# Performance work log

Measured on AMD Instinct MI355X. Metric: run time of the kernel, lower is better.

The kernel has to match this reference:

```python
import jax, jax.numpy as jnp
import numpy as np

D_MODEL = 1024
D_K = 64
D_V = 64
TEMPERATURE = float(np.sqrt(D_K))
LN_EPS = 1e-5


def setup_inputs() -> dict:
    key = jax.random.key(0)
    ks = jax.random.split(key, 8)
    B, L = 8, 2048
    q = jax.random.normal(ks[0], (B, L, D_K), dtype=jnp.float32)
    k = jax.random.normal(ks[1], (B, L, D_K), dtype=jnp.float32)
    v = jax.random.normal(ks[2], (B, L, D_V), dtype=jnp.float32)
    residual = jax.random.normal(ks[3], (B, L, D_MODEL), dtype=jnp.float32)
    # fc: Linear(d_v, d_model), xavier-normal weight, zero-ish bias
    fc_w = jax.random.normal(ks[4], (D_MODEL, D_V), dtype=jnp.float32) * float(np.sqrt(2.0 / (D_V + D_MODEL)))
    fc_b = jnp.zeros((D_MODEL,), dtype=jnp.float32)
    ln_gamma = jnp.ones((D_MODEL,), dtype=jnp.float32)
    ln_beta = jnp.zeros((D_MODEL,), dtype=jnp.float32)
    return {"q": q, "k": k, "v": v, "residual": residual,
            "fc_w": fc_w, "fc_b": fc_b, "ln_gamma": ln_gamma, "ln_beta": ln_beta}


def reference(q, k, v, residual, fc_w, fc_b, ln_gamma, ln_beta):
    # scaled dot-product attention: scores [B, Lq, Lk]
    scores = jnp.einsum("bqd,bkd->bqk", q, k) / TEMPERATURE
    # module computes both log_softmax and softmax (shared logsumexp in a
    # fused kernel); log_attn is discarded by Attention.forward
    log_attn = jax.nn.log_softmax(scores, axis=2)
    attn = jnp.exp(log_attn)  # == softmax(scores); dropout is identity at eval
    out = jnp.einsum("bqk,bkv->bqv", attn, v)  # [B, Lq, d_v]
    # fc + residual + LayerNorm (dropout identity at eval)
    out = jnp.einsum("bqv,mv->bqm", out, fc_w) + fc_b
    x = out + residual
    mu = jnp.mean(x, axis=-1, keepdims=True)
    var = jnp.var(x, axis=-1, keepdims=True)
    return (x - mu) * jax.lax.rsqrt(var + LN_EPS) * ln_gamma + ln_beta
```

## Files before the change

kernel.cpp:

```cpp
#include <hip/hip_runtime.h>

typedef float  f32x4 __attribute__((ext_vector_type(4)));
typedef float  f4v   __attribute__((ext_vector_type(4)));
typedef short  s16x8 __attribute__((ext_vector_type(8)));
typedef unsigned short u16x4 __attribute__((ext_vector_type(4)));
typedef unsigned short u16x8 __attribute__((ext_vector_type(8)));
typedef unsigned short u16;

#define DEVI static __device__ __forceinline__
#define AS1 __attribute__((address_space(1)))
#define AS3 __attribute__((address_space(3)))

DEVI u16 f2bf(float f) {
  unsigned int u = __builtin_bit_cast(unsigned int, f);
  u += 0x7FFFu + ((u >> 16) & 1u);
  return (u16)(u >> 16);
}

constexpr int B  = 8;
constexpr int L  = 2048;
constexpr int D  = 64;
constexpr int DM = 1024;

__global__ void prep_kernel(const float* __restrict__ k, const float* __restrict__ v,
                            const float* __restrict__ w,
                            u16* __restrict__ kbf, u16* __restrict__ vtbf,
                            u16* __restrict__ wbf) {
  __shared__ float tile[64 * 65];
  const int bid = blockIdx.x, tid = threadIdx.x;
  if (bid < 1024) {
    const int i = bid * 256 + tid;
    f4v f = ((const f4v*)k)[i];
    u16x4 o;
#pragma unroll
    for (int j = 0; j < 4; ++j) o[j] = f2bf(f[j] * 0.125f);
    ((u16x4*)kbf)[i] = o;
  } else if (bid < 1024 + 64) {
    const int i = (bid - 1024) * 256 + tid;
    f4v f = ((const f4v*)w)[i];
    u16x4 o;
#pragma unroll
    for (int j = 0; j < 4; ++j) o[j] = f2bf(f[j]);
    ((u16x4*)wbf)[i] = o;
  } else {
    const int t2 = bid - 1088;
    const int b = t2 >> 5, tt = t2 & 31;
    const float* vp = v + ((size_t)b * L + tt * 64) * D;
    for (int i = tid; i < 4096; i += 256) {
      const int r = i >> 6, c = i & 63;
      tile[c * 65 + r] = vp[i];
    }
    __syncthreads();
    u16* op = vtbf + (size_t)b * D * L + tt * 64;
    for (int i = tid; i < 4096; i += 256) {
      const int dv = i >> 6, kv = i & 63;
      op[(size_t)dv * L + kv] = f2bf(tile[dv * 65 + kv]);
    }
  }
}

__global__ __launch_bounds__(512) void attn_kernel(const float* __restrict__ q,
                                                   const u16* __restrict__ kbf,
                                                   const u16* __restrict__ vtbf,
                                                   u16* __restrict__ Og) {
  const int blk = blockIdx.x;
  const int b = blk >> 5;
  const int qrow0 = (blk & 31) * 64;
  const int tid = threadIdx.x;
  const int wave = tid >> 6, lane = tid & 63;
  const int g = wave >> 1, h = wave & 1;
  const int lg = lane >> 4, ln = lane & 15;

  __shared__ __align__(16) u16   Kt[2][64 * 64];
  __shared__ __align__(16) u16   Vt[2][64 * 64];
  __shared__ __align__(16) u16   Pl[8][16 * 40];
  __shared__ float Macc[8][16][68];
  __shared__ float Lsum[8][16];

  s16x8 aq[2];
  {
    const float* qp = q + ((size_t)b * L + qrow0 + g * 16 + ln) * D + lg * 8;
#pragma unroll
    for (int kk = 0; kk < 2; ++kk) {
      f4v f0 = *(const f4v*)(qp + kk * 32);
      f4v f1 = *(const f4v*)(qp + kk * 32 + 4);
      s16x8 a;
#pragma unroll
      for (int j = 0; j < 4; ++j) { a[j] = (short)f2bf(f0[j]); a[4 + j] = (short)f2bf(f1[j]); }
      aq[kk] = a;
    }
  }

  const f32x4 zf = {0.f, 0.f, 0.f, 0.f};
  f32x4 acc[4];
#pragma unroll
  for (int i = 0; i < 4; ++i) acc[i] = zf;
  float lrow[4] = {0.f, 0.f, 0.f, 0.f};

  const u16* kb = kbf + (size_t)b * L * D;
  const u16* vb = vtbf + (size_t)b * D * L;

  auto stage = [&](int buf, int t) {
    const int kv0 = t * 64;
    const int row = tid >> 3, jl = tid & 7;
    const int js = jl ^ (row & 7);
    const u16* srcK = kb + (size_t)(kv0 + row) * D + js * 8;
    __builtin_amdgcn_global_load_lds(
        (const AS1 unsigned int*)srcK, (AS3 unsigned int*)&Kt[buf][tid * 8], 16, 0, 0);
    const u16* srcV = vb + (size_t)row * L + kv0 + js * 8;
    __builtin_amdgcn_global_load_lds(
        (const AS1 unsigned int*)srcV, (AS3 unsigned int*)&Vt[buf][tid * 8], 16, 0, 0);
  };

  stage(0, 0);

  for (int t = 0; t < 32; ++t) {
    __syncthreads();
    if (t + 1 < 32) stage((t + 1) & 1, t + 1);
    const int buf = t & 1;

    f32x4 s[2];
    s[0] = zf; s[1] = zf;
#pragma unroll
    for (int kk = 0; kk < 2; ++kk) {
#pragma unroll
      for (int fn2 = 0; fn2 < 2; ++fn2) {
        const int kvr = h * 32 + fn2 * 16 + ln;
        const int j = (kk * 4 + lg) ^ (kvr & 7);
        s16x8 bk = *(const s16x8*)&Kt[buf][kvr * 64 + j * 8];
        s[fn2] = __builtin_amdgcn_mfma_f32_16x16x32_bf16(aq[kk], bk, s[fn2], 0, 0, 0);
      }
    }

#pragma unroll
    for (int r = 0; r < 4; ++r) {
      const float p0 = __expf(s[0][r]);
      const float p1 = __expf(s[1][r]);
      lrow[r] += p0 + p1;
      Pl[wave][(lg * 4 + r) * 40 + ln]      = f2bf(p0);
      Pl[wave][(lg * 4 + r) * 40 + 16 + ln] = f2bf(p1);
    }

    asm volatile("" ::: "memory");

    s16x8 ap = *(const s16x8*)&Pl[wave][ln * 40 + lg * 8];
#pragma unroll
    for (int fn = 0; fn < 4; ++fn) {
      const int dv = fn * 16 + ln;
      const int j = (h * 4 + lg) ^ (dv & 7);
      s16x8 bv = *(const s16x8*)&Vt[buf][dv * 64 + j * 8];
      acc[fn] = __builtin_amdgcn_mfma_f32_16x16x32_bf16(ap, bv, acc[fn], 0, 0, 0);
    }
  }

#pragma unroll
  for (int r = 0; r < 4; ++r) {
#pragma unroll
    for (int off = 1; off < 16; off <<= 1) lrow[r] += __shfl_xor(lrow[r], off, 64);
    if (ln == 0) Lsum[wave][lg * 4 + r] = lrow[r];
  }
#pragma unroll
  for (int fn = 0; fn < 4; ++fn)
#pragma unroll
    for (int r = 0; r < 4; ++r)
      Macc[wave][lg * 4 + r][fn * 16 + ln] = acc[fn][r];
  __syncthreads();

  {
    const int row = tid >> 3, d0 = (tid & 7) * 8;
    const int g2 = row >> 4, r2 = row & 15;
    const float linv = 1.f / (Lsum[g2 * 2][r2] + Lsum[g2 * 2 + 1][r2]);
    f4v o0 = *(const f4v*)&Macc[g2 * 2][r2][d0]     + *(const f4v*)&Macc[g2 * 2 + 1][r2][d0];
    f4v o1 = *(const f4v*)&Macc[g2 * 2][r2][d0 + 4] + *(const f4v*)&Macc[g2 * 2 + 1][r2][d0 + 4];
    u16x8 ob;
#pragma unroll
    for (int j = 0; j < 4; ++j) {
      ob[j]     = f2bf(o0[j] * linv);
      ob[4 + j] = f2bf(o1[j] * linv);
    }
    *(u16x8*)(Og + ((size_t)b * L + qrow0 + row) * D + d0) = ob;
  }
}

__global__ __launch_bounds__(512, 2) void fc_ln_kernel(const u16* __restrict__ Og,
                                                       const u16* __restrict__ wbf,
                                                       const float* __restrict__ bias,
                                                       const float* __restrict__ resid,
                                                       const float* __restrict__ gamma,
                                                       const float* __restrict__ beta,
                                                       float* __restrict__ out) {
  __shared__ __align__(16) u16   Wl[1024 * 64];
  __shared__ __align__(16) float bl[1024];
  __shared__ __align__(16) float gl[1024];
  __shared__ __align__(16) float btl[1024];
  __shared__ float part[8][16][2];

  const int tid = threadIdx.x;
  const int wave = tid >> 6, lane = tid & 63;
  const int rg = wave >> 2, mq = wave & 3;
  const int lg = lane >> 4, ln = lane & 15;
  const int m0 = mq * 256;
  const int rowA = blockIdx.x * 64 + rg * 16 + ln;
  const int rowB = rowA + 32;
  const int jb = ln & 7;

  {
#pragma unroll
    for (int i = 0; i < 16; ++i) {
      const int c = tid + i * 512;
      const int r = c >> 3, j = c & 7;
      const u16* src = wbf + r * 64 + (j ^ (r & 7)) * 8;
      __builtin_amdgcn_global_load_lds(
          (const AS1 unsigned int*)src, (AS3 unsigned int*)&Wl[c * 8], 16, 0, 0);
    }
    if (tid < 256) {
      __builtin_amdgcn_global_load_lds(
          (const AS1 unsigned int*)(bias + tid * 4), (AS3 unsigned int*)&bl[tid * 4], 16, 0, 0);
      __builtin_amdgcn_global_load_lds(
          (const AS1 unsigned int*)(beta + tid * 4), (AS3 unsigned int*)&btl[tid * 4], 16, 0, 0);
    } else {
      const int t2 = tid - 256;
      __builtin_amdgcn_global_load_lds(
          (const AS1 unsigned int*)(gamma + t2 * 4), (AS3 unsigned int*)&gl[t2 * 4], 16, 0, 0);
    }
  }

  f4v boAr0, boAr1;
  {
    const u16* opA = Og + (size_t)rowA * D + lg * 8;
    asm volatile("global_load_dwordx4 %0, %1, off"           : "=v"(boAr0) : "v"(opA) : "memory");
    asm volatile("global_load_dwordx4 %0, %1, off offset:64" : "=v"(boAr1) : "v"(opA) : "memory");
  }
  f4v rsdA[16];
  {
    const float* rp = resid + (size_t)rowA * DM + m0 + lg * 4;
#pragma unroll
    for (int fn = 0; fn < 16; ++fn)
      asm volatile("global_load_dwordx4 %0, %1, off offset:%c2"
                   : "=v"(rsdA[fn]) : "v"(rp), "i"(fn * 64) : "memory");
  }

  asm volatile("s_waitcnt vmcnt(0)" ::: "memory");
  __builtin_amdgcn_sched_barrier(0);
  __builtin_amdgcn_s_barrier();
  __builtin_amdgcn_sched_barrier(0);

  f32x4 acc[16];
#pragma unroll
  for (int fn = 0; fn < 16; ++fn)
    acc[fn] = *(const f4v*)&bl[m0 + fn * 16 + lg * 4] + rsdA[fn];

  f4v boBr0, boBr1;
  {
    const u16* opB = Og + (size_t)rowB * D + lg * 8;
    asm volatile("global_load_dwordx4 %0, %1, off"           : "=v"(boBr0) : "v"(opB) : "memory");
    asm volatile("global_load_dwordx4 %0, %1, off offset:64" : "=v"(boBr1) : "v"(opB) : "memory");
  }
  f4v rsdB[16];
  {
    const float* rp = resid + (size_t)rowB * DM + m0 + lg * 4;
#pragma unroll
    for (int fn = 0; fn < 16; ++fn)
      asm volatile("global_load_dwordx4 %0, %1, off offset:%c2"
                   : "=v"(rsdB[fn]) : "v"(rp), "i"(fn * 64) : "memory");
  }

  {
    const s16x8 bo0 = __builtin_bit_cast(s16x8, boAr0);
    const s16x8 bo1 = __builtin_bit_cast(s16x8, boAr1);
#pragma unroll
    for (int fn = 0; fn < 16; ++fn) {
      const int m = m0 + fn * 16 + ln;
      s16x8 aw0 = *(const s16x8*)&Wl[m * 64 + (lg ^ jb) * 8];
      s16x8 aw1 = *(const s16x8*)&Wl[m * 64 + ((4 + lg) ^ jb) * 8];
      acc[fn] = __builtin_amdgcn_mfma_f32_16x16x32_bf16(aw0, bo0, acc[fn], 0, 0, 0);
      acc[fn] = __builtin_amdgcn_mfma_f32_16x16x32_bf16(aw1, bo1, acc[fn], 0, 0, 0);
    }
    float sum = 0.f, ssq = 0.f;
#pragma unroll
    for (int fn = 0; fn < 16; ++fn)
#pragma unroll
      for (int r = 0; r < 4; ++r) { const float x = acc[fn][r]; sum += x; ssq += x * x; }
    sum += __shfl_xor(sum, 16, 64); ssq += __shfl_xor(ssq, 16, 64);
    sum += __shfl_xor(sum, 32, 64); ssq += __shfl_xor(ssq, 32, 64);
    if (lg == 0) { part[wave][ln][0] = sum; part[wave][ln][1] = ssq; }
    asm volatile("s_waitcnt lgkmcnt(0)" ::: "memory");
    __builtin_amdgcn_s_barrier();
    __builtin_amdgcn_sched_barrier(0);
    float sm = 0.f, q2 = 0.f;
#pragma unroll
    for (int w2 = 0; w2 < 4; ++w2) { sm += part[rg * 4 + w2][ln][0]; q2 += part[rg * 4 + w2][ln][1]; }
    const float mu   = sm * (1.0f / 1024.0f);
    const float var  = q2 * (1.0f / 1024.0f) - mu * mu;
    const float rstd = rsqrtf(var + 1e-5f);
#pragma unroll
    for (int fn = 0; fn < 16; ++fn) {
      const int m4 = m0 + fn * 16 + lg * 4;
      const f4v gm = *(const f4v*)&gl[m4];
      const f4v bt = *(const f4v*)&btl[m4];
      f4v o;
#pragma unroll
      for (int r = 0; r < 4; ++r) o[r] = (acc[fn][r] - mu) * rstd * gm[r] + bt[r];
      *(f4v*)&out[(size_t)rowA * DM + m4] = o;
    }
  }

  asm volatile("s_waitcnt vmcnt(0)" ::: "memory");
  __builtin_amdgcn_sched_barrier(0);
  __builtin_amdgcn_s_barrier();
  __builtin_amdgcn_sched_barrier(0);

  {
#pragma unroll
    for (int fn = 0; fn < 16; ++fn)
      acc[fn] = *(const f4v*)&bl[m0 + fn * 16 + lg * 4] + rsdB[fn];
    const s16x8 bo0 = __builtin_bit_cast(s16x8, boBr0);
    const s16x8 bo1 = __builtin_bit_cast(s16x8, boBr1);
#pragma unroll
    for (int fn = 0; fn < 16; ++fn) {
      const int m = m0 + fn * 16 + ln;
      s16x8 aw0 = *(const s16x8*)&Wl[m * 64 + (lg ^ jb) * 8];
      s16x8 aw1 = *(const s16x8*)&Wl[m * 64 + ((4 + lg) ^ jb) * 8];
      acc[fn] = __builtin_amdgcn_mfma_f32_16x16x32_bf16(aw0, bo0, acc[fn], 0, 0, 0);
      acc[fn] = __builtin_amdgcn_mfma_f32_16x16x32_bf16(aw1, bo1, acc[fn], 0, 0, 0);
    }
    float sum = 0.f, ssq = 0.f;
#pragma unroll
    for (int fn = 0; fn < 16; ++fn)
#pragma unroll
      for (int r = 0; r < 4; ++r) { const float x = acc[fn][r]; sum += x; ssq += x * x; }
    sum += __shfl_xor(sum, 16, 64); ssq += __shfl_xor(ssq, 16, 64);
    sum += __shfl_xor(sum, 32, 64); ssq += __shfl_xor(ssq, 32, 64);
    if (lg == 0) { part[wave][ln][0] = sum; part[wave][ln][1] = ssq; }
    asm volatile("s_waitcnt lgkmcnt(0)" ::: "memory");
    __builtin_amdgcn_s_barrier();
    __builtin_amdgcn_sched_barrier(0);
    float sm = 0.f, q2 = 0.f;
#pragma unroll
    for (int w2 = 0; w2 < 4; ++w2) { sm += part[rg * 4 + w2][ln][0]; q2 += part[rg * 4 + w2][ln][1]; }
    const float mu   = sm * (1.0f / 1024.0f);
    const float var  = q2 * (1.0f / 1024.0f) - mu * mu;
    const float rstd = rsqrtf(var + 1e-5f);
#pragma unroll
    for (int fn = 0; fn < 16; ++fn) {
      const int m4 = m0 + fn * 16 + lg * 4;
      const f4v gm = *(const f4v*)&gl[m4];
      const f4v bt = *(const f4v*)&btl[m4];
      f4v o;
#pragma unroll
      for (int r = 0; r < 4; ++r) o[r] = (acc[fn][r] - mu) * rstd * gm[r] + bt[r];
      *(f4v*)&out[(size_t)rowB * DM + m4] = o;
    }
  }
}

extern "C" void kernel_launch(void* const* d_in, const int* in_sizes, int n_in,
                              void* d_out, int out_size, void* d_ws, size_t ws_size,
                              hipStream_t stream) {
  const float* q     = (const float*)d_in[0];
  const float* k     = (const float*)d_in[1];
  const float* v     = (const float*)d_in[2];
  const float* resid = (const float*)d_in[3];
  const float* fc_w  = (const float*)d_in[4];
  const float* fc_b  = (const float*)d_in[5];
  const float* gamma = (const float*)d_in[6];
  const float* beta  = (const float*)d_in[7];
  float* out = (float*)d_out;

  char* ws = (char*)d_ws;
  u16*   kbf  = (u16*)(ws);
  u16*   vtbf = (u16*)(ws + (2u << 20));
  u16*   wbf  = (u16*)(ws + (4u << 20));
  u16*   Og   = (u16*)(ws + (4u << 20) + (128u << 10));

  prep_kernel<<<1344, 256, 0, stream>>>(k, v, fc_w, kbf, vtbf, wbf);
  attn_kernel<<<256, 512, 0, stream>>>(q, kbf, vtbf, Og);
  fc_ln_kernel<<<256, 512, 0, stream>>>(Og, wbf, fc_b, resid, gamma, beta, out);
}
```

Measured before the change: 64.13 us.

## Triple-buffer K/V tiles with vmcnt waits and alias epilogue LDS

Moves the attention kernel's K/V staging from a double buffer to a triple buffer that prefetches two tiles ahead. Each iteration waits on vmcnt and a raw s_barrier, so the wait covers only the older loads rather than a full __syncthreads. The epilogue Macc/Lsum scratch is aliased over the K/V buffers in one shared byte array to keep LDS usage near 58 KB. This aims to hide global load latency better, but relies on hand-written vmcnt counts matching the issued loads, and the extra barrier before the epilogue guards the aliasing.

```diff
diff --git a/kernel.cpp b/kernel.cpp
--- a/kernel.cpp
+++ b/kernel.cpp
@@ -63,6 +63,13 @@
                                                    const u16* __restrict__ kbf,
                                                    const u16* __restrict__ vtbf,
                                                    u16* __restrict__ Og) {
+  __shared__ __align__(16) char smem[58 * 1024];
+  u16*   Kt   = (u16*)smem;
+  u16*   Vt   = (u16*)(smem + 24 * 1024);
+  u16*   Pl   = (u16*)(smem + 48 * 1024);
+  float* Macc = (float*)smem;
+  float* Lsum = (float*)(smem + 35 * 1024);
+
   const int blk = blockIdx.x;
   const int b = blk >> 5;
   const int qrow0 = (blk & 31) * 64;
@@ -71,12 +78,6 @@
   const int g = wave >> 1, h = wave & 1;
   const int lg = lane >> 4, ln = lane & 15;
 
-  __shared__ __align__(16) u16   Kt[2][64 * 64];
-  __shared__ __align__(16) u16   Vt[2][64 * 64];
-  __shared__ __align__(16) u16   Pl[8][16 * 40];
-  __shared__ float Macc[8][16][68];
-  __shared__ float Lsum[8][16];
-
   s16x8 aq[2];
   {
     const float* qp = q + ((size_t)b * L + qrow0 + g * 16 + ln) * D + lg * 8;
@@ -100,24 +101,30 @@
   const u16* kb = kbf + (size_t)b * L * D;
   const u16* vb = vtbf + (size_t)b * D * L;
 
-  auto stage = [&](int buf, int t) {
+  auto stage = [&](int t) {
+    const int buf = t % 3;
     const int kv0 = t * 64;
     const int row = tid >> 3, jl = tid & 7;
     const int js = jl ^ (row & 7);
     const u16* srcK = kb + (size_t)(kv0 + row) * D + js * 8;
     __builtin_amdgcn_global_load_lds(
-        (const AS1 unsigned int*)srcK, (AS3 unsigned int*)&Kt[buf][tid * 8], 16, 0, 0);
+        (const AS1 unsigned int*)srcK, (AS3 unsigned int*)&Kt[buf * 4096 + tid * 8], 16, 0, 0);
     const u16* srcV = vb + (size_t)row * L + kv0 + js * 8;
     __builtin_amdgcn_global_load_lds(
-        (const AS1 unsigned int*)srcV, (AS3 unsigned int*)&Vt[buf][tid * 8], 16, 0, 0);
+        (const AS1 unsigned int*)srcV, (AS3 unsigned int*)&Vt[buf * 4096 + tid * 8], 16, 0, 0);
   };
 
-  stage(0, 0);
+  stage(0);
+  stage(1);
 
   for (int t = 0; t < 32; ++t) {
-    __syncthreads();
-    if (t + 1 < 32) stage((t + 1) & 1, t + 1);
-    const int buf = t & 1;
+    if (t < 31) { asm volatile("s_waitcnt vmcnt(2)" ::: "memory"); }
+    else        { asm volatile("s_waitcnt vmcnt(0)" ::: "memory"); }
+    __builtin_amdgcn_sched_barrier(0);
+    __builtin_amdgcn_s_barrier();
+    __builtin_amdgcn_sched_barrier(0);
+    if (t + 2 < 32) stage(t + 2);
+    const int buf = t % 3;
 
     f32x4 s[2];
     s[0] = zf; s[1] = zf;
@@ -127,7 +134,7 @@
       for (int fn2 = 0; fn2 < 2; ++fn2) {
         const int kvr = h * 32 + fn2 * 16 + ln;
         const int j = (kk * 4 + lg) ^ (kvr & 7);
-        s16x8 bk = *(const s16x8*)&Kt[buf][kvr * 64 + j * 8];
+        s16x8 bk = *(const s16x8*)&Kt[buf * 4096 + kvr * 64 + j * 8];
         s[fn2] = __builtin_amdgcn_mfma_f32_16x16x32_bf16(aq[kk], bk, s[fn2], 0, 0, 0);
       }
     }
@@ -137,41 +144,45 @@
       const float p0 = __expf(s[0][r]);
       const float p1 = __expf(s[1][r]);
       lrow[r] += p0 + p1;
-      Pl[wave][(lg * 4 + r) * 40 + ln]      = f2bf(p0);
-      Pl[wave][(lg * 4 + r) * 40 + 16 + ln] = f2bf(p1);
+      Pl[wave * 640 + (lg * 4 + r) * 40 + ln]      = f2bf(p0);
+      Pl[wave * 640 + (lg * 4 + r) * 40 + 16 + ln] = f2bf(p1);
     }
 
     asm volatile("" ::: "memory");
 
-    s16x8 ap = *(const s16x8*)&Pl[wave][ln * 40 + lg * 8];
+    s16x8 ap = *(const s16x8*)&Pl[wave * 640 + ln * 40 + lg * 8];
 #pragma unroll
     for (int fn = 0; fn < 4; ++fn) {
       const int dv = fn * 16 + ln;
       const int j = (h * 4 + lg) ^ (dv & 7);
-      s16x8 bv = *(const s16x8*)&Vt[buf][dv * 64 + j * 8];
+      s16x8 bv = *(const s16x8*)&Vt[buf * 4096 + dv * 64 + j * 8];
       acc[fn] = __builtin_amdgcn_mfma_f32_16x16x32_bf16(ap, bv, acc[fn], 0, 0, 0);
     }
   }
 
+  __syncthreads();
+
 #pragma unroll
   for (int r = 0; r < 4; ++r) {
 #pragma unroll
     for (int off = 1; off < 16; off <<= 1) lrow[r] += __shfl_xor(lrow[r], off, 64);
-    if (ln == 0) Lsum[wave][lg * 4 + r] = lrow[r];
+    if (ln == 0) Lsum[wave * 16 + lg * 4 + r] = lrow[r];
   }
 #pragma unroll
   for (int fn = 0; fn < 4; ++fn)
 #pragma unroll
     for (int r = 0; r < 4; ++r)
-      Macc[wave][lg * 4 + r][fn * 16 + ln] = acc[fn][r];
+      Macc[wave * 1088 + (lg * 4 + r) * 68 + fn * 16 + ln] = acc[fn][r];
   __syncthreads();
 
   {
     const int row = tid >> 3, d0 = (tid & 7) * 8;
     const int g2 = row >> 4, r2 = row & 15;
-    const float linv = 1.f / (Lsum[g2 * 2][r2] + Lsum[g2 * 2 + 1][r2]);
-    f4v o0 = *(const f4v*)&Macc[g2 * 2][r2][d0]     + *(const f4v*)&Macc[g2 * 2 + 1][r2][d0];
-    f4v o1 = *(const f4v*)&Macc[g2 * 2][r2][d0 + 4] + *(const f4v*)&Macc[g2 * 2 + 1][r2][d0 + 4];
+    const float linv = 1.f / (Lsum[(g2 * 2) * 16 + r2] + Lsum[(g2 * 2 + 1) * 16 + r2]);
+    const float* m0p = &Macc[(g2 * 2) * 1088 + r2 * 68 + d0];
+    const float* m1p = &Macc[(g2 * 2 + 1) * 1088 + r2 * 68 + d0];
+    f4v o0 = *(const f4v*)(m0p)     + *(const f4v*)(m1p);
+    f4v o1 = *(const f4v*)(m0p + 4) + *(const f4v*)(m1p + 4);
     u16x8 ob;
 #pragma unroll
     for (int j = 0; j < 4; ++j) {
```

New measurement: 59.19 us. 7.7% less time.
